# Performance work log

Hardware: AMD Instinct MI355X
Metric: run time of the kernel (lower is better)

## Reference

```python
import jax, jax.numpy as jnp
import numpy as np

B, N = 8, 64          # batch, keywords per utterance
D = 768               # audio/transformer d_model
T = 512               # CLIP text embedding dim
V = 49408             # CLIP BPE vocab size
TAU = 0.1             # VQ softmax temperature
EPS = 1e-8            # cosine-similarity eps (matches F.cosine_similarity)


def setup_inputs() -> dict:
    key = jax.random.key(0)
    k1, k2, k3 = jax.random.split(key, 3)
    return {
        "audio_feat": jax.random.normal(k1, (B, N, D), dtype=jnp.float32),
        "W_proj": jax.random.normal(k2, (D, T), dtype=jnp.float32) * 0.02,
        "b_proj": jnp.zeros((T,), dtype=jnp.float32),
        "token_emb": jax.random.normal(k3, (V, T), dtype=jnp.float32) * 0.02,
    }


def _l2_normalize(x, axis):
    n = jnp.sqrt(jnp.sum(x * x, axis=axis, keepdims=True))
    return x / jnp.maximum(n, EPS)


def reference(audio_feat, W_proj, b_proj, token_emb):
    # project_feats_to_CLIPspace: linear projection d_model -> text_dim
    kw = jnp.einsum("bnd,dt->bnt", audio_feat, W_proj) + b_proj  # [B,N,T]

    # get_keyword_cosine_score: cosine sim vs full CLIP vocab, expressed as
    # one normalized GEMM instead of the per-keyword broadcast loop.
    kw_n = _l2_normalize(kw, axis=-1)            # [B,N,T]
    emb_n = _l2_normalize(token_emb, axis=-1)    # [V,T]
    cos_score = jnp.einsum("bnt,vt->bnv", kw_n, emb_n)  # [B,N,V]

    # vector quantizer: straight-through hard selection over the vocab
    prob = jax.nn.softmax(cos_score / TAU, axis=-1)              # [B,N,V]
    hard = jax.nn.one_hot(jnp.argmax(cos_score, axis=-1), V,
                          dtype=cos_score.dtype)                  # [B,N,V]
    subword_prob = hard + prob - jax.lax.stop_gradient(prob)

    # keywords = subword_prob @ frozen token embedding table
    keywords = jnp.einsum("bnv,vt->bnt", subword_prob, token_emb)  # [B,N,T]
    return keywords
```

## Files before the change

### kernel.cpp

```cpp
#include <hip/hip_runtime.h>

constexpr int M_ROWS = 512;
constexpr int D_IN   = 768;
constexpr int T_DIM  = 512;
constexpr int V_SIZE = 49408;
constexpr int NV32   = V_SIZE / 32;
constexpr int NK16   = T_DIM / 16;
constexpr float EPS  = 1e-8f;

typedef short bf16x8 __attribute__((ext_vector_type(8)));
typedef float f32x16 __attribute__((ext_vector_type(16)));

__device__ inline unsigned short bf16_rne(float f) {
  unsigned int u = __float_as_uint(f);
  u += 0x7FFFu + ((u >> 16) & 1u);
  return (unsigned short)(u >> 16);
}
__device__ inline float bf16_f32(unsigned short h) {
  return __uint_as_float(((unsigned int)h) << 16);
}
__device__ inline unsigned int f32_sortable(float f) {
  unsigned int u = __float_as_uint(f);
  return (u & 0x80000000u) ? ~u : (u | 0x80000000u);
}
__device__ inline unsigned long long shfl_xor_u64(unsigned long long x, int mask) {
  unsigned int lo = (unsigned int)(x & 0xFFFFFFFFull);
  unsigned int hi = (unsigned int)(x >> 32);
  lo = __shfl_xor(lo, mask);
  hi = __shfl_xor(hi, mask);
  return ((unsigned long long)hi << 32) | (unsigned long long)lo;
}

__device__ inline size_t frag_idx(int tile_slot, int rc, int k) {
  return (size_t)tile_slot * 512 +
         (size_t)(((rc & 31) | (((k >> 3) & 1) << 5)) * 8) + (k & 7);
}

template <int FRAG>
__global__ __launch_bounds__(256) void proj_kernel(
    const float* __restrict__ audio, const float* __restrict__ W,
    const float* __restrict__ bias, unsigned short* __restrict__ kwH,
    unsigned short* __restrict__ kwL) {
  __shared__ float a[4][D_IN];
  const int tid = threadIdx.x;
  const int m0 = blockIdx.x * 4;

  const float4* src4 = reinterpret_cast<const float4*>(audio + (size_t)m0 * D_IN);
  float4* a4 = reinterpret_cast<float4*>(&a[0][0]);
  #pragma unroll
  for (int i = 0; i < 3; ++i) a4[tid + 256 * i] = src4[tid + 256 * i];
  __syncthreads();

  const int t0 = tid, t1 = tid + 256;
  float acc[4][2] = {};
  #pragma unroll 4
  for (int d = 0; d < D_IN; ++d) {
    const float w0 = W[(size_t)d * T_DIM + t0];
    const float w1 = W[(size_t)d * T_DIM + t1];
    #pragma unroll
    for (int r = 0; r < 4; ++r) {
      acc[r][0] = fmaf(a[r][d], w0, acc[r][0]);
      acc[r][1] = fmaf(a[r][d], w1, acc[r][1]);
    }
  }
  const float b0 = bias[t0], b1 = bias[t1];
  #pragma unroll
  for (int r = 0; r < 4; ++r) {
    const int row = m0 + r;
    const float v0 = acc[r][0] + b0;
    const float v1 = acc[r][1] + b1;
    const unsigned short h0 = bf16_rne(v0);
    const unsigned short h1 = bf16_rne(v1);
    const unsigned short l0 = bf16_rne(v0 - bf16_f32(h0));
    const unsigned short l1 = bf16_rne(v1 - bf16_f32(h1));
    if (FRAG) {
      const size_t i0 = frag_idx((row >> 5) * NK16 + (t0 >> 4), row, t0);
      const size_t i1 = frag_idx((row >> 5) * NK16 + (t1 >> 4), row, t1);
      kwH[i0] = h0; kwH[i1] = h1;
      kwL[i0] = l0; kwL[i1] = l1;
    } else {
      kwH[(size_t)row * T_DIM + t0] = h0;
      kwH[(size_t)row * T_DIM + t1] = h1;
      kwL[(size_t)row * T_DIM + t0] = l0;
      kwL[(size_t)row * T_DIM + t1] = l1;
    }
  }
}

__global__ __launch_bounds__(256) void split_kernel(
    const float* __restrict__ emb, unsigned short* __restrict__ embHf,
    unsigned short* __restrict__ embLf) {
  __shared__ float lds_inv[32];
  const int tid = threadIdx.x;
  const int v0 = blockIdx.x * 32;

  {
    const float* rp = emb + (size_t)(v0 + (tid >> 3)) * T_DIM + (tid & 7) * 64;
    const float4* rp4 = reinterpret_cast<const float4*>(rp);
    float ss = 0.0f;
    #pragma unroll
    for (int i = 0; i < 16; ++i) {
      const float4 x = rp4[i];
      ss += x.x * x.x + x.y * x.y + x.z * x.z + x.w * x.w;
    }
    ss += __shfl_xor(ss, 1);
    ss += __shfl_xor(ss, 2);
    ss += __shfl_xor(ss, 4);
    if ((tid & 7) == 0) lds_inv[tid >> 3] = 1.0f / fmaxf(sqrtf(ss), EPS);
  }
  __syncthreads();

  const int w = tid >> 6, l = tid & 63;
  const float s = lds_inv[l & 31];
  const size_t gbase = (size_t)(v0 + (l & 31)) * T_DIM + (l >> 5) * 8;
  const size_t obase = (size_t)blockIdx.x * 32 * 512 + (size_t)l * 8;
  #pragma unroll
  for (int i = 0; i < 8; ++i) {
    const int k16 = w * 8 + i;
    const float4 x0 = *reinterpret_cast<const float4*>(&emb[gbase + k16 * 16]);
    const float4 x1 = *reinterpret_cast<const float4*>(&emb[gbase + k16 * 16 + 4]);
    const float xv[8] = {x0.x, x0.y, x0.z, x0.w, x1.x, x1.y, x1.z, x1.w};
    bf16x8 hv, lv;
    #pragma unroll
    for (int j = 0; j < 8; ++j) {
      const float x = xv[j] * s;
      const unsigned short h = bf16_rne(x);
      hv[j] = (short)h;
      lv[j] = (short)bf16_rne(x - bf16_f32(h));
    }
    *reinterpret_cast<bf16x8*>(&embHf[obase + (size_t)k16 * 512]) = hv;
    *reinterpret_cast<bf16x8*>(&embLf[obase + (size_t)k16 * 512]) = lv;
  }
}

__global__ __launch_bounds__(256, 4) void score_kernel(
    const unsigned short* __restrict__ kwHf, const unsigned short* __restrict__ kwLf,
    const unsigned short* __restrict__ embHf, const unsigned short* __restrict__ embLf,
    unsigned long long* __restrict__ best) {
  __shared__ short ldsB[2][2][4][2][512];

  const int tid  = threadIdx.x;
  const int lane = tid & 63;
  const int w    = tid >> 6;
  const int xb   = blockIdx.x;
  const int m0   = blockIdx.y * 128;

  const unsigned short* gp[4];
  int ldsOff[4];
  #pragma unroll
  for (int q = 0; q < 4; ++q) {
    const int idx = w * 4 + q;
    const int hl = idx & 1, k16o = (idx >> 1) & 1, v32o = idx >> 2;
    const unsigned short* src = hl ? embLf : embHf;
    gp[q] = src + ((size_t)(xb * 4 + v32o) * NK16 + k16o) * 512 + (size_t)lane * 8;
    ldsOff[q] = ((k16o * 4 + v32o) * 2 + hl) * 512 + lane * 8;
  }

  const unsigned short* aHp =
      kwHf + (size_t)((m0 >> 5) + w) * NK16 * 512 + (size_t)lane * 8;
  const unsigned short* aLp =
      kwLf + (size_t)((m0 >> 5) + w) * NK16 * 512 + (size_t)lane * 8;

  f32x16 acc[4];
  #pragma unroll
  for (int ct = 0; ct < 4; ++ct)
    #pragma unroll
    for (int i = 0; i < 16; ++i) acc[ct][i] = 0.0f;

  bf16x8 sreg[4];

  #pragma unroll
  for (int q = 0; q < 4; ++q) sreg[q] = *reinterpret_cast<const bf16x8*>(gp[q]);
  {
    short* b0 = &ldsB[0][0][0][0][0];
    #pragma unroll
    for (int q = 0; q < 4; ++q)
      *reinterpret_cast<bf16x8*>(b0 + ldsOff[q]) = sreg[q];
  }
  __syncthreads();

  for (int ci = 0; ci < 16; ++ci) {
    const int buf = ci & 1;

    if (ci < 15) {
      #pragma unroll
      for (int q = 0; q < 4; ++q)
        sreg[q] = *reinterpret_cast<const bf16x8*>(gp[q] + (size_t)(ci + 1) * 1024);
    }

    bf16x8 aH[2], aL[2];
    #pragma unroll
    for (int ks = 0; ks < 2; ++ks) {
      aH[ks] = *reinterpret_cast<const bf16x8*>(aHp + (size_t)(ci * 2 + ks) * 512);
      aL[ks] = *reinterpret_cast<const bf16x8*>(aLp + (size_t)(ci * 2 + ks) * 512);
    }

    const short* bb = &ldsB[buf][0][0][0][0];
    #pragma unroll
    for (int ks = 0; ks < 2; ++ks) {
      #pragma unroll
      for (int ct = 0; ct < 4; ++ct) {
        const bf16x8 bH = *reinterpret_cast<const bf16x8*>(
            bb + ((ks * 4 + ct) * 2 + 0) * 512 + lane * 8);
        const bf16x8 bL = *reinterpret_cast<const bf16x8*>(
            bb + ((ks * 4 + ct) * 2 + 1) * 512 + lane * 8);
        acc[ct] = __builtin_amdgcn_mfma_f32_32x32x16_bf16(aH[ks], bH, acc[ct], 0, 0, 0);
        acc[ct] = __builtin_amdgcn_mfma_f32_32x32x16_bf16(aH[ks], bL, acc[ct], 0, 0, 0);
        acc[ct] = __builtin_amdgcn_mfma_f32_32x32x16_bf16(aL[ks], bH, acc[ct], 0, 0, 0);
      }
    }

    if (ci < 15) {
      short* bn = &ldsB[buf ^ 1][0][0][0][0];
      #pragma unroll
      for (int q = 0; q < 4; ++q)
        *reinterpret_cast<bf16x8*>(bn + ldsOff[q]) = sreg[q];
    }
    __syncthreads();
  }

  const int rowbase = m0 + w * 32 + 4 * (lane >> 5);
  #pragma unroll
  for (int reg = 0; reg < 16; ++reg) {
    const int row = rowbase + (reg & 3) + 8 * (reg >> 2);
    unsigned long long pk = 0;
    #pragma unroll
    for (int ct = 0; ct < 4; ++ct) {
      const float s = acc[ct][reg];
      const unsigned long long p =
          ((unsigned long long)f32_sortable(s) << 32) |
          (unsigned long long)(0xFFFFFFFFu - (unsigned)(xb * 128 + ct * 32 + (lane & 31)));
      if (p > pk) pk = p;
    }
    #pragma unroll
    for (int off = 1; off < 32; off <<= 1) {
      const unsigned long long o = shfl_xor_u64(pk, off);
      if (o > pk) pk = o;
    }
    if ((lane & 31) == 0) atomicMax(&best[row], pk);
  }
}

__global__ __launch_bounds__(256) void norm_kernel(
    const float* __restrict__ emb, float* __restrict__ inv_norm) {
  const int wave = threadIdx.x >> 6;
  const int lane = threadIdx.x & 63;
  const int v = blockIdx.x * 4 + wave;
  const float4* row = reinterpret_cast<const float4*>(emb + (size_t)v * T_DIM);
  const float4 x = row[lane];
  const float4 y = row[lane + 64];
  float ss = x.x * x.x + x.y * x.y + x.z * x.z + x.w * x.w +
             y.x * y.x + y.y * y.y + y.z * y.z + y.w * y.w;
  #pragma unroll
  for (int off = 32; off > 0; off >>= 1) ss += __shfl_xor(ss, off);
  if (lane == 0) inv_norm[v] = 1.0f / fmaxf(sqrtf(ss), EPS);
}

__global__ __launch_bounds__(256, 2) void score_v1_kernel(
    const unsigned short* __restrict__ kwH, const unsigned short* __restrict__ kwL,
    const float* __restrict__ emb, const float* __restrict__ inv_norm,
    unsigned long long* __restrict__ best) {
  __shared__ short ldsH[2][8][64][8];
  __shared__ short ldsL[2][8][64][8];
  const int tid  = threadIdx.x;
  const int lane = tid & 63;
  const int w    = tid >> 6;
  const int n0   = blockIdx.x * 128;
  const int m0   = blockIdx.y * 256;
  size_t sg[2]; float ssc[2]; int sof[2];
  #pragma unroll
  for (int p = 0; p < 2; ++p) {
    const int s  = tid + 256 * p;
    const int ls = s & 63;
    const int nt = (s >> 6) & 3;
    const int ks = (s >> 8) & 1;
    const int col  = nt * 32 + (ls & 31);
    const int krel = ks * 16 + (ls >> 5) * 8;
    sg[p]  = (size_t)(n0 + col) * T_DIM + krel;
    ssc[p] = inv_norm[n0 + col];
    sof[p] = ((ks * 4 + nt) * 64 + ls) * 8;
  }
  const int kh = (lane >> 5) * 8;
  size_t aOff[2];
  #pragma unroll
  for (int rt = 0; rt < 2; ++rt)
    aOff[rt] = (size_t)(m0 + w * 64 + rt * 32 + (lane & 31)) * T_DIM + kh;
  f32x16 acc[2][4];
  #pragma unroll
  for (int rt = 0; rt < 2; ++rt)
    #pragma unroll
    for (int ct = 0; ct < 4; ++ct)
      #pragma unroll
      for (int i = 0; i < 16; ++i) acc[rt][ct][i] = 0.0f;
  float ld[2][8];
  #pragma unroll
  for (int p = 0; p < 2; ++p) {
    const float4 x0 = *reinterpret_cast<const float4*>(&emb[sg[p]]);
    const float4 x1 = *reinterpret_cast<const float4*>(&emb[sg[p] + 4]);
    ld[p][0] = x0.x; ld[p][1] = x0.y; ld[p][2] = x0.z; ld[p][3] = x0.w;
    ld[p][4] = x1.x; ld[p][5] = x1.y; ld[p][6] = x1.z; ld[p][7] = x1.w;
  }
  {
    short* hw = &ldsH[0][0][0][0];
    short* lw = &ldsL[0][0][0][0];
    #pragma unroll
    for (int p = 0; p < 2; ++p) {
      bf16x8 hv, lv;
      #pragma unroll
      for (int j = 0; j < 8; ++j) {
        const float x = ld[p][j] * ssc[p];
        const unsigned short h = bf16_rne(x);
        hv[j] = (short)h;
        lv[j] = (short)bf16_rne(x - bf16_f32(h));
      }
      *reinterpret_cast<bf16x8*>(hw + sof[p]) = hv;
      *reinterpret_cast<bf16x8*>(lw + sof[p]) = lv;
    }
  }
  __syncthreads();
  for (int ci = 0; ci < 16; ++ci) {
    const int buf = ci & 1;
    if (ci < 15) {
      #pragma unroll
      for (int p = 0; p < 2; ++p) {
        const size_t g = sg[p] + (size_t)(ci + 1) * 32;
        const float4 x0 = *reinterpret_cast<const float4*>(&emb[g]);
        const float4 x1 = *reinterpret_cast<const float4*>(&emb[g + 4]);
        ld[p][0] = x0.x; ld[p][1] = x0.y; ld[p][2] = x0.z; ld[p][3] = x0.w;
        ld[p][4] = x1.x; ld[p][5] = x1.y; ld[p][6] = x1.z; ld[p][7] = x1.w;
      }
    }
    const short* hq = &ldsH[buf][0][0][0];
    const short* lq = &ldsL[buf][0][0][0];
    #pragma unroll
    for (int ks = 0; ks < 2; ++ks) {
      const size_t ak = (size_t)(ci * 32 + ks * 16);
      bf16x8 aH[2], aL[2];
      #pragma unroll
      for (int rt = 0; rt < 2; ++rt) {
        aH[rt] = *reinterpret_cast<const bf16x8*>(&kwH[aOff[rt] + ak]);
        aL[rt] = *reinterpret_cast<const bf16x8*>(&kwL[aOff[rt] + ak]);
      }
      #pragma unroll
      for (int ct = 0; ct < 4; ++ct) {
        const bf16x8 bH = *reinterpret_cast<const bf16x8*>(hq + ((ks * 4 + ct) * 64 + lane) * 8);
        const bf16x8 bL = *reinterpret_cast<const bf16x8*>(lq + ((ks * 4 + ct) * 64 + lane) * 8);
        #pragma unroll
        for (int rt = 0; rt < 2; ++rt) {
          acc[rt][ct] = __builtin_amdgcn_mfma_f32_32x32x16_bf16(aH[rt], bH, acc[rt][ct], 0, 0, 0);
          acc[rt][ct] = __builtin_amdgcn_mfma_f32_32x32x16_bf16(aH[rt], bL, acc[rt][ct], 0, 0, 0);
          acc[rt][ct] = __builtin_amdgcn_mfma_f32_32x32x16_bf16(aL[rt], bH, acc[rt][ct], 0, 0, 0);
        }
      }
    }
    if (ci < 15) {
      short* hw = &ldsH[buf ^ 1][0][0][0];
      short* lw = &ldsL[buf ^ 1][0][0][0];
      #pragma unroll
      for (int p = 0; p < 2; ++p) {
        bf16x8 hv, lv;
        #pragma unroll
        for (int j = 0; j < 8; ++j) {
          const float x = ld[p][j] * ssc[p];
          const unsigned short h = bf16_rne(x);
          hv[j] = (short)h;
          lv[j] = (short)bf16_rne(x - bf16_f32(h));
        }
        *reinterpret_cast<bf16x8*>(hw + sof[p]) = hv;
        *reinterpret_cast<bf16x8*>(lw + sof[p]) = lv;
      }
    }
    __syncthreads();
  }
  #pragma unroll
  for (int rt = 0; rt < 2; ++rt) {
    const int rowbase = m0 + w * 64 + rt * 32 + 4 * (lane >> 5);
    #pragma unroll
    for (int reg = 0; reg < 16; ++reg) {
      const int row = rowbase + (reg & 3) + 8 * (reg >> 2);
      unsigned long long pk = 0;
      #pragma unroll
      for (int ct = 0; ct < 4; ++ct) {
        const float s = acc[rt][ct][reg];
        const unsigned long long p =
            ((unsigned long long)f32_sortable(s) << 32) |
            (unsigned long long)(0xFFFFFFFFu - (unsigned)(n0 + ct * 32 + (lane & 31)));
        if (p > pk) pk = p;
      }
      #pragma unroll
      for (int off = 1; off < 32; off <<= 1) {
        const unsigned long long o = shfl_xor_u64(pk, off);
        if (o > pk) pk = o;
      }
      if ((lane & 31) == 0) atomicMax(&best[row], pk);
    }
  }
}

__global__ __launch_bounds__(128) void gather_kernel(
    const float* __restrict__ emb, const unsigned long long* __restrict__ best,
    float* __restrict__ out) {
  const int row = blockIdx.x;
  const unsigned int idx =
      0xFFFFFFFFu - (unsigned int)(best[row] & 0xFFFFFFFFull);
  const float4* src = reinterpret_cast<const float4*>(emb + (size_t)idx * T_DIM);
  float4* dst = reinterpret_cast<float4*>(out + (size_t)row * T_DIM);
  dst[threadIdx.x] = src[threadIdx.x];
}

extern "C" void kernel_launch(void* const* d_in, const int* in_sizes, int n_in,
                              void* d_out, int out_size, void* d_ws, size_t ws_size,
                              hipStream_t stream) {
  const float* audio = (const float*)d_in[0];
  const float* Wp    = (const float*)d_in[1];
  const float* bp    = (const float*)d_in[2];
  const float* emb   = (const float*)d_in[3];
  float* out = (float*)d_out;

  const size_t kw_elems  = (size_t)M_ROWS * T_DIM;
  const size_t emb_elems = (size_t)V_SIZE * T_DIM;
  const size_t need = 2 * kw_elems * 2 + 2 * emb_elems * 2 +
                      M_ROWS * sizeof(unsigned long long);

  char* ws = (char*)d_ws;
  if (ws_size >= need) {
    unsigned short* kwHf  = (unsigned short*)ws;
    unsigned short* kwLf  = kwHf + kw_elems;
    unsigned short* embHf = kwLf + kw_elems;
    unsigned short* embLf = embHf + emb_elems;
    unsigned long long* best = (unsigned long long*)(embLf + emb_elems);

    hipMemsetAsync(best, 0, M_ROWS * sizeof(unsigned long long), stream);
    proj_kernel<1><<<M_ROWS / 4, 256, 0, stream>>>(audio, Wp, bp, kwHf, kwLf);
    split_kernel<<<NV32, 256, 0, stream>>>(emb, embHf, embLf);
    score_kernel<<<dim3(V_SIZE / 128, M_ROWS / 128), 256, 0, stream>>>(
        kwHf, kwLf, embHf, embLf, best);
    gather_kernel<<<M_ROWS, 128, 0, stream>>>(emb, best, out);
  } else {
    unsigned short* kwH = (unsigned short*)ws;
    unsigned short* kwL = kwH + kw_elems;
    float* inv_norm = (float*)(kwL + kw_elems);
    unsigned long long* best = (unsigned long long*)(inv_norm + V_SIZE);

    hipMemsetAsync(best, 0, M_ROWS * sizeof(unsigned long long), stream);
    proj_kernel<0><<<M_ROWS / 4, 256, 0, stream>>>(audio, Wp, bp, kwH, kwL);
    norm_kernel<<<V_SIZE / 4, 256, 0, stream>>>(emb, inv_norm);
    score_v1_kernel<<<dim3(V_SIZE / 128, M_ROWS / 256), 256, 0, stream>>>(
        kwH, kwL, emb, inv_norm, best);
    gather_kernel<<<M_ROWS, 128, 0, stream>>>(emb, best, out);
  }
}
```

Measured before the change: 403.7 us.

## Fuse projection and embedding split into one launch; enlarge score row tile

Projection and embedding-split kernels are merged into one prep kernel that picks its branch by block index, removing a launch and letting the two overlap. The score kernel now handles 256 rows per block with two row tiles per wave, so each LDS-staged embedding tile is reused twice as much. It halves global and LDS reads of the bf16 embedding table. The grid is reordered so the two row blocks sharing an embedding tile are adjacent. The cost is doubled accumulator registers, with launch bounds lowered to 2 blocks per CU and fewer total blocks.

```diff
diff --git a/kernel.cpp b/kernel.cpp
--- a/kernel.cpp
+++ b/kernel.cpp
@@ -34,6 +34,213 @@
 __device__ inline size_t frag_idx(int tile_slot, int rc, int k) {
   return (size_t)tile_slot * 512 +
          (size_t)(((rc & 31) | (((k >> 3) & 1) << 5)) * 8) + (k & 7);
+}
+
+__global__ __launch_bounds__(256) void prep_kernel(
+    const float* __restrict__ audio, const float* __restrict__ W,
+    const float* __restrict__ bias, unsigned short* __restrict__ kwH,
+    unsigned short* __restrict__ kwL, const float* __restrict__ emb,
+    unsigned short* __restrict__ embHf, unsigned short* __restrict__ embLf) {
+  __shared__ float a[4][D_IN];
+  __shared__ float lds_inv[32];
+  const int tid = threadIdx.x;
+
+  if (blockIdx.x < 128) {
+    const int m0 = blockIdx.x * 4;
+    const float4* src4 = reinterpret_cast<const float4*>(audio + (size_t)m0 * D_IN);
+    float4* a4 = reinterpret_cast<float4*>(&a[0][0]);
+    #pragma unroll
+    for (int i = 0; i < 3; ++i) a4[tid + 256 * i] = src4[tid + 256 * i];
+    __syncthreads();
+
+    const int t0 = tid, t1 = tid + 256;
+    float acc[4][2] = {};
+    #pragma unroll 4
+    for (int d = 0; d < D_IN; ++d) {
+      const float w0 = W[(size_t)d * T_DIM + t0];
+      const float w1 = W[(size_t)d * T_DIM + t1];
+      #pragma unroll
+      for (int r = 0; r < 4; ++r) {
+        acc[r][0] = fmaf(a[r][d], w0, acc[r][0]);
+        acc[r][1] = fmaf(a[r][d], w1, acc[r][1]);
+      }
+    }
+    const float b0 = bias[t0], b1 = bias[t1];
+    #pragma unroll
+    for (int r = 0; r < 4; ++r) {
+      const int row = m0 + r;
+      const float v0 = acc[r][0] + b0;
+      const float v1 = acc[r][1] + b1;
+      const unsigned short h0 = bf16_rne(v0);
+      const unsigned short h1 = bf16_rne(v1);
+      const size_t i0 = frag_idx((row >> 5) * NK16 + (t0 >> 4), row, t0);
+      const size_t i1 = frag_idx((row >> 5) * NK16 + (t1 >> 4), row, t1);
+      kwH[i0] = h0; kwH[i1] = h1;
+      kwL[i0] = bf16_rne(v0 - bf16_f32(h0));
+      kwL[i1] = bf16_rne(v1 - bf16_f32(h1));
+    }
+  } else {
+    const int vb = blockIdx.x - 128;
+    const int v0 = vb * 32;
+
+    {
+      const float* rp = emb + (size_t)(v0 + (tid >> 3)) * T_DIM + (tid & 7) * 64;
+      const float4* rp4 = reinterpret_cast<const float4*>(rp);
+      float ss = 0.0f;
+      #pragma unroll
+      for (int i = 0; i < 16; ++i) {
+        const float4 x = rp4[i];
+        ss += x.x * x.x + x.y * x.y + x.z * x.z + x.w * x.w;
+      }
+      ss += __shfl_xor(ss, 1);
+      ss += __shfl_xor(ss, 2);
+      ss += __shfl_xor(ss, 4);
+      if ((tid & 7) == 0) lds_inv[tid >> 3] = 1.0f / fmaxf(sqrtf(ss), EPS);
+    }
+    __syncthreads();
+
+    const int w = tid >> 6, l = tid & 63;
+    const float s = lds_inv[l & 31];
+    const size_t gbase = (size_t)(v0 + (l & 31)) * T_DIM + (l >> 5) * 8;
+    const size_t obase = (size_t)vb * 32 * 512 + (size_t)l * 8;
+    #pragma unroll
+    for (int i = 0; i < 8; ++i) {
+      const int k16 = w * 8 + i;
+      const float4 x0 = *reinterpret_cast<const float4*>(&emb[gbase + k16 * 16]);
+      const float4 x1 = *reinterpret_cast<const float4*>(&emb[gbase + k16 * 16 + 4]);
+      const float xv[8] = {x0.x, x0.y, x0.z, x0.w, x1.x, x1.y, x1.z, x1.w};
+      bf16x8 hv, lv;
+      #pragma unroll
+      for (int j = 0; j < 8; ++j) {
+        const float x = xv[j] * s;
+        const unsigned short h = bf16_rne(x);
+        hv[j] = (short)h;
+        lv[j] = (short)bf16_rne(x - bf16_f32(h));
+      }
+      *reinterpret_cast<bf16x8*>(&embHf[obase + (size_t)k16 * 512]) = hv;
+      *reinterpret_cast<bf16x8*>(&embLf[obase + (size_t)k16 * 512]) = lv;
+    }
+  }
+}
+
+__global__ __launch_bounds__(256, 2) void score_kernel(
+    const unsigned short* __restrict__ kwHf, const unsigned short* __restrict__ kwLf,
+    const unsigned short* __restrict__ embHf, const unsigned short* __restrict__ embLf,
+    unsigned long long* __restrict__ best) {
+  __shared__ short ldsB[2][16][512];
+
+  const int tid  = threadIdx.x;
+  const int lane = tid & 63;
+  const int w    = tid >> 6;
+  const int m0   = blockIdx.x * 256;
+  const int yb   = blockIdx.y;
+
+  const unsigned short* gp[4];
+  int ldsOff[4];
+  #pragma unroll
+  for (int q = 0; q < 4; ++q) {
+    const int idx = w * 4 + q;
+    const int hl = idx & 1, k16o = (idx >> 1) & 1, v32o = idx >> 2;
+    const unsigned short* src = hl ? embLf : embHf;
+    gp[q] = src + ((size_t)(yb * 4 + v32o) * NK16 + k16o) * 512 + (size_t)lane * 8;
+    ldsOff[q] = ((k16o * 4 + v32o) * 2 + hl) * 512 + lane * 8;
+  }
+
+  const unsigned short* aHp[2];
+  const unsigned short* aLp[2];
+  #pragma unroll
+  for (int rt = 0; rt < 2; ++rt) {
+    const size_t base =
+        (size_t)(blockIdx.x * 8 + w * 2 + rt) * NK16 * 512 + (size_t)lane * 8;
+    aHp[rt] = kwHf + base;
+    aLp[rt] = kwLf + base;
+  }
+
+  f32x16 acc[2][4];
+  #pragma unroll
+  for (int rt = 0; rt < 2; ++rt)
+    #pragma unroll
+    for (int ct = 0; ct < 4; ++ct)
+      #pragma unroll
+      for (int i = 0; i < 16; ++i) acc[rt][ct][i] = 0.0f;
+
+  bf16x8 sreg[4];
+
+  #pragma unroll
+  for (int q = 0; q < 4; ++q) sreg[q] = *reinterpret_cast<const bf16x8*>(gp[q]);
+  {
+    short* b0 = &ldsB[0][0][0];
+    #pragma unroll
+    for (int q = 0; q < 4; ++q)
+      *reinterpret_cast<bf16x8*>(b0 + ldsOff[q]) = sreg[q];
+  }
+  __syncthreads();
+
+  for (int ci = 0; ci < 16; ++ci) {
+    const int buf = ci & 1;
+
+    if (ci < 15) {
+      #pragma unroll
+      for (int q = 0; q < 4; ++q)
+        sreg[q] = *reinterpret_cast<const bf16x8*>(gp[q] + (size_t)(ci + 1) * 1024);
+    }
+
+    const short* bb = &ldsB[buf][0][0];
+    #pragma unroll
+    for (int ks = 0; ks < 2; ++ks) {
+      bf16x8 aH[2], aL[2];
+      #pragma unroll
+      for (int rt = 0; rt < 2; ++rt) {
+        aH[rt] = *reinterpret_cast<const bf16x8*>(aHp[rt] + (size_t)(ci * 2 + ks) * 512);
+        aL[rt] = *reinterpret_cast<const bf16x8*>(aLp[rt] + (size_t)(ci * 2 + ks) * 512);
+      }
+      #pragma unroll
+      for (int ct = 0; ct < 4; ++ct) {
+        const bf16x8 bH = *reinterpret_cast<const bf16x8*>(
+            bb + ((ks * 4 + ct) * 2 + 0) * 512 + lane * 8);
+        const bf16x8 bL = *reinterpret_cast<const bf16x8*>(
+            bb + ((ks * 4 + ct) * 2 + 1) * 512 + lane * 8);
+        #pragma unroll
+        for (int rt = 0; rt < 2; ++rt) {
+          acc[rt][ct] = __builtin_amdgcn_mfma_f32_32x32x16_bf16(aH[rt], bH, acc[rt][ct], 0, 0, 0);
+          acc[rt][ct] = __builtin_amdgcn_mfma_f32_32x32x16_bf16(aH[rt], bL, acc[rt][ct], 0, 0, 0);
+          acc[rt][ct] = __builtin_amdgcn_mfma_f32_32x32x16_bf16(aL[rt], bH, acc[rt][ct], 0, 0, 0);
+        }
+      }
+    }
+
+    if (ci < 15) {
+      short* bn = &ldsB[buf ^ 1][0][0];
+      #pragma unroll
+      for (int q = 0; q < 4; ++q)
+        *reinterpret_cast<bf16x8*>(bn + ldsOff[q]) = sreg[q];
+    }
+    __syncthreads();
+  }
+
+  #pragma unroll
+  for (int rt = 0; rt < 2; ++rt) {
+    const int rowbase = m0 + w * 64 + rt * 32 + 4 * (lane >> 5);
+    #pragma unroll
+    for (int reg = 0; reg < 16; ++reg) {
+      const int row = rowbase + (reg & 3) + 8 * (reg >> 2);
+      unsigned long long pk = 0;
+      #pragma unroll
+      for (int ct = 0; ct < 4; ++ct) {
+        const float s = acc[rt][ct][reg];
+        const unsigned long long p =
+            ((unsigned long long)f32_sortable(s) << 32) |
+            (unsigned long long)(0xFFFFFFFFu - (unsigned)(yb * 128 + ct * 32 + (lane & 31)));
+        if (p > pk) pk = p;
+      }
+      #pragma unroll
+      for (int off = 1; off < 32; off <<= 1) {
+        const unsigned long long o = shfl_xor_u64(pk, off);
+        if (o > pk) pk = o;
+      }
+      if ((lane & 31) == 0) atomicMax(&best[row], pk);
+    }
+  }
 }
 
 template <int FRAG>
@@ -44,13 +251,11 @@
   __shared__ float a[4][D_IN];
   const int tid = threadIdx.x;
   const int m0 = blockIdx.x * 4;
-
   const float4* src4 = reinterpret_cast<const float4*>(audio + (size_t)m0 * D_IN);
   float4* a4 = reinterpret_cast<float4*>(&a[0][0]);
   #pragma unroll
   for (int i = 0; i < 3; ++i) a4[tid + 256 * i] = src4[tid + 256 * i];
   __syncthreads();
-
   const int t0 = tid, t1 = tid + 256;
   float acc[4][2] = {};
   #pragma unroll 4
@@ -71,173 +276,18 @@
     const float v1 = acc[r][1] + b1;
     const unsigned short h0 = bf16_rne(v0);
     const unsigned short h1 = bf16_rne(v1);
-    const unsigned short l0 = bf16_rne(v0 - bf16_f32(h0));
-    const unsigned short l1 = bf16_rne(v1 - bf16_f32(h1));
     if (FRAG) {
       const size_t i0 = frag_idx((row >> 5) * NK16 + (t0 >> 4), row, t0);
       const size_t i1 = frag_idx((row >> 5) * NK16 + (t1 >> 4), row, t1);
       kwH[i0] = h0; kwH[i1] = h1;
-      kwL[i0] = l0; kwL[i1] = l1;
+      kwL[i0] = bf16_rne(v0 - bf16_f32(h0));
+      kwL[i1] = bf16_rne(v1 - bf16_f32(h1));
     } else {
       kwH[(size_t)row * T_DIM + t0] = h0;
       kwH[(size_t)row * T_DIM + t1] = h1;
-      kwL[(size_t)row * T_DIM + t0] = l0;
-      kwL[(size_t)row * T_DIM + t1] = l1;
-    }
-  }
-}
-
-__global__ __launch_bounds__(256) void split_kernel(
-    const float* __restrict__ emb, unsigned short* __restrict__ embHf,
-    unsigned short* __restrict__ embLf) {
-  __shared__ float lds_inv[32];
-  const int tid = threadIdx.x;
-  const int v0 = blockIdx.x * 32;
-
-  {
-    const float* rp = emb + (size_t)(v0 + (tid >> 3)) * T_DIM + (tid & 7) * 64;
-    const float4* rp4 = reinterpret_cast<const float4*>(rp);
-    float ss = 0.0f;
-    #pragma unroll
-    for (int i = 0; i < 16; ++i) {
-      const float4 x = rp4[i];
-      ss += x.x * x.x + x.y * x.y + x.z * x.z + x.w * x.w;
-    }
-    ss += __shfl_xor(ss, 1);
-    ss += __shfl_xor(ss, 2);
-    ss += __shfl_xor(ss, 4);
-    if ((tid & 7) == 0) lds_inv[tid >> 3] = 1.0f / fmaxf(sqrtf(ss), EPS);
-  }
-  __syncthreads();
-
-  const int w = tid >> 6, l = tid & 63;
-  const float s = lds_inv[l & 31];
-  const size_t gbase = (size_t)(v0 + (l & 31)) * T_DIM + (l >> 5) * 8;
-  const size_t obase = (size_t)blockIdx.x * 32 * 512 + (size_t)l * 8;
-  #pragma unroll
-  for (int i = 0; i < 8; ++i) {
-    const int k16 = w * 8 + i;
-    const float4 x0 = *reinterpret_cast<const float4*>(&emb[gbase + k16 * 16]);
-    const float4 x1 = *reinterpret_cast<const float4*>(&emb[gbase + k16 * 16 + 4]);
-    const float xv[8] = {x0.x, x0.y, x0.z, x0.w, x1.x, x1.y, x1.z, x1.w};
-    bf16x8 hv, lv;
-    #pragma unroll
-    for (int j = 0; j < 8; ++j) {
-      const float x = xv[j] * s;
-      const unsigned short h = bf16_rne(x);
-      hv[j] = (short)h;
-      lv[j] = (short)bf16_rne(x - bf16_f32(h));
-    }
-    *reinterpret_cast<bf16x8*>(&embHf[obase + (size_t)k16 * 512]) = hv;
-    *reinterpret_cast<bf16x8*>(&embLf[obase + (size_t)k16 * 512]) = lv;
-  }
-}
-
-__global__ __launch_bounds__(256, 4) void score_kernel(
-    const unsigned short* __restrict__ kwHf, const unsigned short* __restrict__ kwLf,
-    const unsigned short* __restrict__ embHf, const unsigned short* __restrict__ embLf,
-    unsigned long long* __restrict__ best) {
-  __shared__ short ldsB[2][2][4][2][512];
-
-  const int tid  = threadIdx.x;
-  const int lane = tid & 63;
-  const int w    = tid >> 6;
-  const int xb   = blockIdx.x;
-  const int m0   = blockIdx.y * 128;
-
-  const unsigned short* gp[4];
-  int ldsOff[4];
-  #pragma unroll
-  for (int q = 0; q < 4; ++q) {
-    const int idx = w * 4 + q;
-    const int hl = idx & 1, k16o = (idx >> 1) & 1, v32o = idx >> 2;
-    const unsigned short* src = hl ? embLf : embHf;
-    gp[q] = src + ((size_t)(xb * 4 + v32o) * NK16 + k16o) * 512 + (size_t)lane * 8;
-    ldsOff[q] = ((k16o * 4 + v32o) * 2 + hl) * 512 + lane * 8;
-  }
-
-  const unsigned short* aHp =
-      kwHf + (size_t)((m0 >> 5) + w) * NK16 * 512 + (size_t)lane * 8;
-  const unsigned short* aLp =
-      kwLf + (size_t)((m0 >> 5) + w) * NK16 * 512 + (size_t)lane * 8;
-
-  f32x16 acc[4];
-  #pragma unroll
-  for (int ct = 0; ct < 4; ++ct)
-    #pragma unroll
-    for (int i = 0; i < 16; ++i) acc[ct][i] = 0.0f;
-
-  bf16x8 sreg[4];
-
-  #pragma unroll
-  for (int q = 0; q < 4; ++q) sreg[q] = *reinterpret_cast<const bf16x8*>(gp[q]);
-  {
-    short* b0 = &ldsB[0][0][0][0][0];
-    #pragma unroll
-    for (int q = 0; q < 4; ++q)
-      *reinterpret_cast<bf16x8*>(b0 + ldsOff[q]) = sreg[q];
-  }
-  __syncthreads();
-
-  for (int ci = 0; ci < 16; ++ci) {
-    const int buf = ci & 1;
-
-    if (ci < 15) {
-      #pragma unroll
-      for (int q = 0; q < 4; ++q)
-        sreg[q] = *reinterpret_cast<const bf16x8*>(gp[q] + (size_t)(ci + 1) * 1024);
-    }
-
-    bf16x8 aH[2], aL[2];
-    #pragma unroll
-    for (int ks = 0; ks < 2; ++ks) {
-      aH[ks] = *reinterpret_cast<const bf16x8*>(aHp + (size_t)(ci * 2 + ks) * 512);
-      aL[ks] = *reinterpret_cast<const bf16x8*>(aLp + (size_t)(ci * 2 + ks) * 512);
-    }
-
-    const short* bb = &ldsB[buf][0][0][0][0];
-    #pragma unroll
-    for (int ks = 0; ks < 2; ++ks) {
-      #pragma unroll
-      for (int ct = 0; ct < 4; ++ct) {
-        const bf16x8 bH = *reinterpret_cast<const bf16x8*>(
-            bb + ((ks * 4 + ct) * 2 + 0) * 512 + lane * 8);
-        const bf16x8 bL = *reinterpret_cast<const bf16x8*>(
-            bb + ((ks * 4 + ct) * 2 + 1) * 512 + lane * 8);
-        acc[ct] = __builtin_amdgcn_mfma_f32_32x32x16_bf16(aH[ks], bH, acc[ct], 0, 0, 0);
-        acc[ct] = __builtin_amdgcn_mfma_f32_32x32x16_bf16(aH[ks], bL, acc[ct], 0, 0, 0);
-        acc[ct] = __builtin_amdgcn_mfma_f32_32x32x16_bf16(aL[ks], bH, acc[ct], 0, 0, 0);
-      }
-    }
-
-    if (ci < 15) {
-      short* bn = &ldsB[buf ^ 1][0][0][0][0];
-      #pragma unroll
-      for (int q = 0; q < 4; ++q)
-        *reinterpret_cast<bf16x8*>(bn + ldsOff[q]) = sreg[q];
-    }
-    __syncthreads();
-  }
-
-  const int rowbase = m0 + w * 32 + 4 * (lane >> 5);
-  #pragma unroll
-  for (int reg = 0; reg < 16; ++reg) {
-    const int row = rowbase + (reg & 3) + 8 * (reg >> 2);
-    unsigned long long pk = 0;
-    #pragma unroll
-    for (int ct = 0; ct < 4; ++ct) {
-      const float s = acc[ct][reg];
-      const unsigned long long p =
-          ((unsigned long long)f32_sortable(s) << 32) |
-          (unsigned long long)(0xFFFFFFFFu - (unsigned)(xb * 128 + ct * 32 + (lane & 31)));
-      if (p > pk) pk = p;
-    }
-    #pragma unroll
-    for (int off = 1; off < 32; off <<= 1) {
-      const unsigned long long o = shfl_xor_u64(pk, off);
-      if (o > pk) pk = o;
-    }
-    if ((lane & 31) == 0) atomicMax(&best[row], pk);
+      kwL[(size_t)row * T_DIM + t0] = bf16_rne(v0 - bf16_f32(h0));
+      kwL[(size_t)row * T_DIM + t1] = bf16_rne(v1 - bf16_f32(h1));
+    }
   }
 }
 
@@ -431,9 +481,9 @@
     unsigned long long* best = (unsigned long long*)(embLf + emb_elems);
 
     hipMemsetAsync(best, 0, M_ROWS * sizeof(unsigned long long), stream);
-    proj_kernel<1><<<M_ROWS / 4, 256, 0, stream>>>(audio, Wp, bp, kwHf, kwLf);
-    split_kernel<<<NV32, 256, 0, stream>>>(emb, embHf, embLf);
-    score_kernel<<<dim3(V_SIZE / 128, M_ROWS / 128), 256, 0, stream>>>(
+    prep_kernel<<<128 + NV32, 256, 0, stream>>>(audio, Wp, bp, kwHf, kwLf,
+                                                emb, embHf, embLf);
+    score_kernel<<<dim3(M_ROWS / 256, V_SIZE / 128), 256, 0, stream>>>(
         kwHf, kwLf, embHf, embLf, best);
     gather_kernel<<<M_ROWS, 128, 0, stream>>>(emb, best, out);
   } else {
```

Result: faster. 371.0 us (-8.1%).
